# Kernel optimization log

Hardware: AMD Instinct MI355X
Metric: run time of the kernel (lower is better)

## Reference

```python
import jax, jax.numpy as jnp
import numpy as np

D_MODEL = 2048
N_HEADS = 16
D_KEY = D_MODEL // N_HEADS
ALIBI_SLOPE = 8.0
KEY_SCALE = D_KEY ** -0.5
B, S = 2, 2048


def setup_inputs() -> dict:
    key = jax.random.key(0)
    ks = jax.random.split(key, 12)
    sd = D_MODEL ** -0.5
    return {
        "states": jax.random.normal(ks[0], (B, S, D_MODEL), jnp.float32),
        "bias_mask": jax.random.normal(ks[1], (B, S, S), jnp.float32),
        # weights stored [in, out] (torch Linear applies x @ W.T + b)
        "wq": jax.random.normal(ks[2], (D_MODEL, D_MODEL), jnp.float32) * sd,
        "bq": jnp.zeros((D_MODEL,), jnp.float32),
        "wk": jax.random.normal(ks[3], (D_MODEL, D_MODEL), jnp.float32) * sd,
        "bk": jnp.zeros((D_MODEL,), jnp.float32),
        "wv": jax.random.normal(ks[4], (D_MODEL, D_MODEL), jnp.float32) * sd,
        "bv": jnp.zeros((D_MODEL,), jnp.float32),
        "wg": jax.random.normal(ks[5], (D_MODEL, N_HEADS), jnp.float32) * sd,
        "bg": jnp.zeros((N_HEADS,), jnp.float32),
        "wo": jax.random.normal(ks[6], (D_MODEL, D_MODEL), jnp.float32) * sd,
        "bo": jnp.zeros((D_MODEL,), jnp.float32),
    }


def reference(states, bias_mask, wq, bq, wk, bk, wv, bv, wg, bg, wo, bo):
    # head_scale = exp2(-(h+1)*alibi_slope/n_heads), non-trainable buffer
    head_scale = jnp.exp2(-(jnp.arange(N_HEADS, dtype=jnp.float32) + 1.0)
                          * ALIBI_SLOPE / N_HEADS)
    # [B, H, Q, K] bias with per-head ALiBi scaling
    bias = bias_mask[:, None, :, :] * head_scale[None, :, None, None]

    def heads(x, w, b):  # [B,S,D] -> [B,H,S,Dk]
        y = x @ w + b
        return y.reshape(x.shape[0], x.shape[1], N_HEADS, D_KEY).transpose(0, 2, 1, 3)

    q = heads(states, wq, bq)
    k = heads(states, wk, bk)
    v = heads(states, wv, bv)

    scores = jnp.einsum('bhqd,bhkd->bhqk', q, k) * KEY_SCALE + bias
    probs = jax.nn.softmax(scores, axis=-1)
    o = jnp.einsum('bhqk,bhkd->bqhd', probs, v)  # [B,S,H,Dk]

    g = jax.nn.sigmoid(states @ wg + bg)  # [B,S,H] head gate
    o = o * g[..., None]

    return o.reshape(o.shape[0], o.shape[1], D_MODEL) @ wo + bo
```

## Files before the change

### kernel.cpp

```cpp
#include <hip/hip_runtime.h>
#include <hip/hip_bf16.h>

#define SEQ 2048
#define DM 2048
#define NH 16
#define DK 128
#define LOG2E 1.4426950408889634f
#define QK_SCALE 0.08838834764831845f

typedef __attribute__((ext_vector_type(8))) short short8;
typedef __attribute__((ext_vector_type(4))) float f32x4;
typedef __attribute__((ext_vector_type(4))) unsigned short us4;

__device__ __forceinline__ unsigned short f2b(float f) {
  union { float f; unsigned u; } v; v.f = f;
  unsigned r = v.u + 0x7fffu + ((v.u >> 16) & 1u);
  return (unsigned short)(r >> 16);
}
__device__ __forceinline__ float b2f(unsigned short v) {
  union { unsigned u; float f; } x; x.u = ((unsigned)v) << 16; return x.f;
}

__device__ __forceinline__ void gl_lds16(const void* g, void* l) {
  __builtin_amdgcn_global_load_lds((const __attribute__((address_space(1))) void*)g,
                                   (__attribute__((address_space(3))) void*)l, 16, 0, 0);
}

#define SBAR()   __builtin_amdgcn_s_barrier()
#define SCHED0() __builtin_amdgcn_sched_barrier(0)
#define LGKM0()  asm volatile("s_waitcnt lgkmcnt(0)" ::: "memory")

__global__ __launch_bounds__(256) void cast2_bf16_kernel(const float* __restrict__ in0,
                                                         unsigned short* __restrict__ out0,
                                                         const float* __restrict__ in1,
                                                         unsigned short* __restrict__ out1) {
  int bid = blockIdx.x;
  const float* in = (bid < 4096) ? in0 : in1;
  unsigned short* out = (bid < 4096) ? out0 : out1;
  int i = ((bid < 4096) ? bid : bid - 4096) * 256 + threadIdx.x;
  const float4* p = (const float4*)in;
  float4 a = p[2*i], b = p[2*i+1];
  us4 r0, r1;
  r0[0]=f2b(a.x); r0[1]=f2b(a.y); r0[2]=f2b(a.z); r0[3]=f2b(a.w);
  r1[0]=f2b(b.x); r1[1]=f2b(b.y); r1[2]=f2b(b.z); r1[3]=f2b(b.w);
  us4* o = (us4*)out;
  o[2*i] = r0; o[2*i+1] = r1;
}

__global__ __launch_bounds__(256) void transpose_cast4_kernel(const float* __restrict__ w0,
                                                              const float* __restrict__ w1,
                                                              const float* __restrict__ w2,
                                                              const float* __restrict__ w3,
                                                              unsigned short* __restrict__ dst) {
  const float* w = (blockIdx.z == 0) ? w0 : (blockIdx.z == 1) ? w1 : (blockIdx.z == 2) ? w2 : w3;
  unsigned short* wt = dst + (size_t)blockIdx.z * DM * DM;
  __shared__ float t[64][65];
  int c0 = blockIdx.x * 64, r0 = blockIdx.y * 64;
  int tid = threadIdx.x;
  int rr = tid >> 4;
  int c4 = (tid & 15) * 4;
#pragma unroll
  for (int p = 0; p < 4; ++p) {
    int r = p*16 + rr;
    float4 v = *(const float4*)&w[(size_t)(r0 + r)*DM + c0 + c4];
    t[r][c4] = v.x; t[r][c4+1] = v.y; t[r][c4+2] = v.z; t[r][c4+3] = v.w;
  }
  __syncthreads();
#pragma unroll
  for (int p = 0; p < 4; ++p) {
    int c = p*16 + rr;
    us4 v;
    v[0] = f2b(t[c4+0][c]); v[1] = f2b(t[c4+1][c]);
    v[2] = f2b(t[c4+2][c]); v[3] = f2b(t[c4+3][c]);
    *(us4*)&wt[(size_t)(c0 + c)*DM + r0 + c4] = v;
  }
}

__global__ __launch_bounds__(256) void transpose_wg_kernel(const float* __restrict__ wg,
                                                           unsigned short* __restrict__ wgT) {
  int idx = blockIdx.x * 256 + threadIdx.x;
  int c = idx & 15;
  int r0 = (idx >> 4) * 4;
#pragma unroll
  for (int r = 0; r < 4; ++r)
    wgT[(size_t)c*DM + r0 + r] = f2b(wg[(size_t)(r0 + r)*NH + c]);
}

__device__ __forceinline__ void gemm128x128_core(const unsigned short* __restrict__ A,
                                                 const unsigned short* __restrict__ Bt,
                                                 int m0, int n0, f32x4 (&acc)[4][4]) {
  __shared__ __align__(16) unsigned short Ab[2][8192];
  __shared__ __align__(16) unsigned short Bb[2][8192];
  const int TK = DM / 64;

  int tid = threadIdx.x, wid = tid >> 6, lane = tid & 63;
  int lo = lane & 15, hi = lane >> 4;
  int wm = wid >> 1, wn = wid & 1;

  int srow8 = lane >> 3;
  int skb = (((lane & 7) ^ srow8) << 4);
  const char* Ag = (const char*)A;
  const char* Bg = (const char*)Bt;

#define STG_A(S,CUR) do {                                                          \
    const char* g = Ag + (size_t)(S)*128 + skb;                                    \
    char* l = (char*)&Ab[CUR][0] + wid*4096;                                       \
    _Pragma("unroll")                                                              \
    for (int c = 0; c < 4; ++c)                                                    \
      gl_lds16(g + (size_t)(m0 + wid*32 + c*8 + srow8)*4096, l + c*1024);          \
  } while(0)
#define STG_B(S,CUR) do {                                                          \
    const char* g = Bg + (size_t)(S)*128 + skb;                                    \
    char* l = (char*)&Bb[CUR][0] + wid*4096;                                       \
    _Pragma("unroll")                                                              \
    for (int c = 0; c < 4; ++c)                                                    \
      gl_lds16(g + (size_t)(n0 + wid*32 + c*8 + srow8)*4096, l + c*1024);          \
  } while(0)

#pragma unroll
  for (int i = 0; i < 4; ++i)
#pragma unroll
    for (int j = 0; j < 4; ++j) acc[i][j] = (f32x4){0.f,0.f,0.f,0.f};

  STG_B(0,0); STG_A(0,0); STG_B(1,1); STG_A(1,1);
  asm volatile("s_waitcnt vmcnt(8)" ::: "memory");
  SBAR();

  int msk = (lo & 7) << 4;
  int k0 = (hi*16) ^ msk;
  int k1 = (64 + hi*16) ^ msk;

  short8 a[4][2], bA[2][2], bB[2][2];

#define MF16(NHH,BF)                                                                \
  __builtin_amdgcn_s_setprio(1);                                                    \
  _Pragma("unroll") for (int mi = 0; mi < 4; ++mi)                                  \
  _Pragma("unroll") for (int nn = 0; nn < 2; ++nn) {                                \
    acc[mi][(NHH)*2+nn] = __builtin_amdgcn_mfma_f32_16x16x32_bf16(                  \
        a[mi][0], BF[nn][0], acc[mi][(NHH)*2+nn], 0, 0, 0);                         \
    acc[mi][(NHH)*2+nn] = __builtin_amdgcn_mfma_f32_16x16x32_bf16(                  \
        a[mi][1], BF[nn][1], acc[mi][(NHH)*2+nn], 0, 0, 0);                         \
  }                                                                                 \
  __builtin_amdgcn_s_setprio(0);

  for (int s = 0; s < TK; ++s) {
    int cur = s & 1;
    const char* Ac = (const char*)&Ab[cur][0];
    const char* Bc = (const char*)&Bb[cur][0];
    bool pre = (s + 2) < TK;

#pragma unroll
    for (int mm = 0; mm < 4; ++mm) {
      a[mm][0] = *(const short8*)(Ac + (wm*64 + mm*16 + lo)*128 + k0);
      a[mm][1] = *(const short8*)(Ac + (wm*64 + mm*16 + lo)*128 + k1);
    }
#pragma unroll
    for (int nn = 0; nn < 2; ++nn) {
      bA[nn][0] = *(const short8*)(Bc + (wn*64 + nn*16 + lo)*128 + k0);
      bA[nn][1] = *(const short8*)(Bc + (wn*64 + nn*16 + lo)*128 + k1);
      bB[nn][0] = *(const short8*)(Bc + (wn*64 + (2+nn)*16 + lo)*128 + k0);
      bB[nn][1] = *(const short8*)(Bc + (wn*64 + (2+nn)*16 + lo)*128 + k1);
    }
    SBAR(); LGKM0(); SCHED0();
    MF16(0, bA);
    SBAR();

    if (pre) {
      STG_B(s + 2, cur);
      STG_A(s + 2, cur);
      asm volatile("s_waitcnt vmcnt(8)" ::: "memory");
    } else if (s == TK - 2) {
      asm volatile("s_waitcnt vmcnt(0)" ::: "memory");
    }
    SBAR();
    MF16(1, bB);
    SBAR();
  }
#undef STG_A
#undef STG_B
#undef MF16
}

__global__ __launch_bounds__(256, 2) void gemm128_qkv_kernel(const unsigned short* __restrict__ A,
                                                             const unsigned short* __restrict__ Bt,
                                                             const float* __restrict__ bq,
                                                             const float* __restrict__ bk,
                                                             const float* __restrict__ bv,
                                                             unsigned short* __restrict__ QB,
                                                             unsigned short* __restrict__ KB,
                                                             unsigned short* __restrict__ VTB) {
  f32x4 acc[4][4];
  int n0 = blockIdx.x * 128, m0 = blockIdx.y * 128;
  gemm128x128_core(A, Bt, m0, n0, acc);

  int tid = threadIdx.x, wid = tid >> 6, lane = tid & 63;
  int lo = lane & 15, hi = lane >> 4;
  int wm = wid >> 1, wn = wid & 1;
  int m_base = m0 + wm*64;
  int n_base = n0 + wn*64;
  int sect = n0 >> 11;

  if (sect == 2) {
#pragma unroll
    for (int mi = 0; mi < 4; ++mi) {
      int m = m_base + mi*16 + 4*hi;
      int b = m >> 11, srow = m & 2047;
#pragma unroll
      for (int nf = 0; nf < 4; ++nf) {
        int n = n_base + nf*16 + lo;
        int nl = n & 2047, h = nl >> 7, d = nl & 127;
        float bvv = bv[nl];
        us4 pk;
#pragma unroll
        for (int r = 0; r < 4; ++r) pk[r] = f2b(acc[mi][nf][r] + bvv);
        *(us4*)&VTB[(((size_t)(b*NH + h))*DK + d)*SEQ + srow] = pk;
      }
    }
  } else {
    unsigned short* out = sect ? KB : QB;
    const float* bp = sect ? bk : bq;
    const float qs = sect ? 1.f : QK_SCALE * LOG2E;
#pragma unroll
    for (int mi = 0; mi < 4; ++mi) {
#pragma unroll
      for (int nf = 0; nf < 4; ++nf) {
        int n = n_base + nf*16 + lo;
        int nl = n & 2047, h = nl >> 7, d = nl & 127;
        float bvv = bp[nl];
#pragma unroll
        for (int r = 0; r < 4; ++r) {
          int m = m_base + mi*16 + 4*hi + r;
          int b = m >> 11, srow = m & 2047;
          out[(((size_t)(b*NH + h))*SEQ + srow)*DK + d] = f2b((acc[mi][nf][r] + bvv) * qs);
        }
      }
    }
  }
}

__global__ __launch_bounds__(256, 2) void gemm128_ao_kernel(const unsigned short* __restrict__ A,
                                                            const unsigned short* __restrict__ Bt,
                                                            const float* __restrict__ bias,
                                                            float* __restrict__ out) {
  f32x4 acc[4][4];
  int n0 = blockIdx.x * 128, m0 = blockIdx.y * 128;
  gemm128x128_core(A, Bt, m0, n0, acc);

  int tid = threadIdx.x, wid = tid >> 6, lane = tid & 63;
  int lo = lane & 15, hi = lane >> 4;
  int wm = wid >> 1, wn = wid & 1;
#pragma unroll
  for (int mi = 0; mi < 4; ++mi) {
#pragma unroll
    for (int nf = 0; nf < 4; ++nf) {
      int n = n0 + wn*64 + nf*16 + lo;
      float bvv = bias[n];
#pragma unroll
      for (int r = 0; r < 4; ++r) {
        int m = m0 + wm*64 + mi*16 + 4*hi + r;
        out[(size_t)m*DM + n] = acc[mi][nf][r] + bvv;
      }
    }
  }
}

__global__ __launch_bounds__(256) void gate_mfma_kernel(const unsigned short* __restrict__ XB,
                                                        const unsigned short* __restrict__ wgT,
                                                        const float* __restrict__ bg,
                                                        float* __restrict__ G) {
  int tid = threadIdx.x, wid = tid >> 6, lane = tid & 63;
  int lo = lane & 15, hi = lane >> 4;
  int m0 = blockIdx.x * 64 + wid * 16;

  f32x4 acc = {0.f, 0.f, 0.f, 0.f};
  const unsigned short* xrow = XB + (size_t)(m0 + lo) * DM + hi * 8;
  const unsigned short* grow = wgT + (size_t)lo * DM + hi * 8;
#pragma unroll 4
  for (int kt = 0; kt < DM; kt += 32) {
    short8 a = *(const short8*)(xrow + kt);
    short8 b = *(const short8*)(grow + kt);
    acc = __builtin_amdgcn_mfma_f32_16x16x32_bf16(a, b, acc, 0, 0, 0);
  }
  float bgv = bg[lo];
#pragma unroll
  for (int r = 0; r < 4; ++r) {
    float x = acc[r] + bgv;
    G[(size_t)(m0 + 4*hi + r) * NH + lo] = 1.f / (1.f + __builtin_amdgcn_exp2f(-x * LOG2E));
  }
}

__global__ __attribute__((amdgpu_flat_work_group_size(512,512)))
__attribute__((amdgpu_waves_per_eu(2,4)))
void attn_kernel(const unsigned short* __restrict__ Q,
                 const unsigned short* __restrict__ Kb,
                 const unsigned short* __restrict__ VT,
                 const unsigned short* __restrict__ biasb,
                 const float* __restrict__ G,
                 unsigned short* __restrict__ OG) {
  __shared__ __align__(16) unsigned short kbuf[2][64*128];
  __shared__ __align__(16) unsigned short vbuf[2][128*64];
  __shared__ __align__(16) unsigned short pbuf[8*16*64];

  int bid = blockIdx.x;
  int h  = bid & 15;
  int b  = (bid >> 4) & 1;
  int qt = bid >> 5;
  int bh = b*NH + h;

  int tid = threadIdx.x, wid = tid >> 6, lane = tid & 63;
  int lo = lane & 15, hi = lane >> 4;
  int qw0 = qt*256 + wid*32;

  float hs2 = __builtin_amdgcn_exp2f(-(float)(h+1) * 0.5f) * LOG2E;

  short8 qf[2][4];
#pragma unroll
  for (int f2 = 0; f2 < 2; ++f2)
#pragma unroll
    for (int ks = 0; ks < 4; ++ks)
      qf[f2][ks] = *(const short8*)&Q[((size_t)bh*SEQ + qw0 + f2*16 + lo)*DK + ks*32 + hi*8];

  f32x4 zero4 = {0.f,0.f,0.f,0.f};
  f32x4 acco[2][8];
#pragma unroll
  for (int f2 = 0; f2 < 2; ++f2)
#pragma unroll
    for (int f = 0; f < 8; ++f) acco[f2][f] = zero4;
  float lrun[2][4];
#pragma unroll
  for (int f2 = 0; f2 < 2; ++f2)
#pragma unroll
    for (int r = 0; r < 4; ++r) lrun[f2][r] = 0.f;

  const char* kbase = (const char*)Kb + ((size_t)bh*SEQ)*DK*2;
  const char* vbase = (const char*)VT + ((size_t)bh*DK)*SEQ*2;
  const unsigned short* bb = biasb + ((size_t)b*SEQ + qw0 + 4*hi)*SEQ + lo;
  char* pb = (char*)pbuf + wid*2048;

  int s16 = lane >> 4, srow8 = lane >> 3;
  int kof = (lane & 15) * 16, vof = (lane & 7) * 16;
  int w2 = wid * 2;

#define STAGE_KV(KT, BUF) do {                                                        \
    _Pragma("unroll")                                                                 \
    for (int c = 0; c < 2; ++c) {                                                     \
      int krc = (w2 + c)*4 + s16;                                                     \
      gl_lds16(kbase + (size_t)((KT) + krc)*256 + (kof ^ ((krc & 7) << 4)),           \
               (char*)kbuf[BUF] + (w2 + c)*1024);                                     \
      int vrc = (w2 + c)*8 + srow8;                                                   \
      gl_lds16(vbase + (size_t)vrc*4096 + (size_t)(KT)*2 + (vof ^ (srow8 << 4)),      \
               (char*)vbuf[BUF] + (w2 + c)*1024);                                     \
    }                                                                                 \
  } while(0)

  unsigned short br[2][4][4];
#pragma unroll
  for (int f2 = 0; f2 < 2; ++f2)
#pragma unroll
    for (int r = 0; r < 4; ++r)
#pragma unroll
      for (int nf = 0; nf < 4; ++nf)
        br[f2][r][nf] = bb[(size_t)(f2*16 + r)*SEQ + nf*16];
  STAGE_KV(0, 0);
  STAGE_KV(64, 1);
  asm volatile("s_waitcnt vmcnt(4)" ::: "memory");
  SBAR();

  const int NT = SEQ / 64;
  int cur = 0;
  for (int t = 0; t < NT; ++t) {
#pragma unroll
    for (int f2 = 0; f2 < 2; ++f2) {
      f32x4 sf[4];
      __builtin_amdgcn_s_setprio(1);
#pragma unroll
      for (int nf = 0; nf < 4; ++nf) {
        f32x4 a = zero4;
#pragma unroll
        for (int ks = 0; ks < 4; ++ks) {
          int krw = nf*16 + lo;
          int cb = (ks*32 + hi*8)*2;
          short8 kf = *(const short8*)((const char*)kbuf[cur] + krw*256 + (cb ^ ((krw & 7) << 4)));
          a = __builtin_amdgcn_mfma_f32_16x16x32_bf16(qf[f2][ks], kf, a, 0, 0, 0);
        }
        sf[nf] = a;
      }
      __builtin_amdgcn_s_setprio(0);

#pragma unroll
      for (int r = 0; r < 4; ++r) {
        int prow = 4*hi + r;
#pragma unroll
        for (int nf = 0; nf < 4; ++nf) {
          float s = fmaf(b2f(br[f2][r][nf]), hs2, sf[nf][r]);
          float p = __builtin_amdgcn_exp2f(s);
          lrun[f2][r] += p;
          *(unsigned short*)(pb + prow*128 + ((((nf*16 + lo)*2)) ^ ((prow & 7) << 4))) = f2b(p);
        }
      }

      short8 pf[2];
#pragma unroll
      for (int ks = 0; ks < 2; ++ks)
        pf[ks] = *(const short8*)(pb + lo*128 + ((ks*64 + hi*16) ^ ((lo & 7) << 4)));
      __builtin_amdgcn_s_setprio(1);
#pragma unroll
      for (int f = 0; f < 8; ++f) {
#pragma unroll
        for (int ks = 0; ks < 2; ++ks) {
          int vrw = f*16 + lo;
          int cb = (ks*32 + hi*8)*2;
          short8 vf = *(const short8*)((const char*)vbuf[cur] + vrw*128 + (cb ^ ((vrw & 7) << 4)));
          acco[f2][f] = __builtin_amdgcn_mfma_f32_16x16x32_bf16(pf[ks], vf, acco[f2][f], 0, 0, 0);
        }
      }
      __builtin_amdgcn_s_setprio(0);
    }

    LGKM0(); SBAR();

    bool more1 = (t + 1) < NT;
    bool more2 = (t + 2) < NT;
    if (more1) {
      int ktn = (t + 1) * 64;
#pragma unroll
      for (int f2 = 0; f2 < 2; ++f2)
#pragma unroll
        for (int r = 0; r < 4; ++r)
#pragma unroll
          for (int nf = 0; nf < 4; ++nf)
            br[f2][r][nf] = bb[(size_t)(f2*16 + r)*SEQ + ktn + nf*16];
    }
    if (more2) {
      STAGE_KV((t + 2) * 64, cur);
      asm volatile("s_waitcnt vmcnt(36)" ::: "memory");
    } else if (more1) {
      asm volatile("s_waitcnt vmcnt(32)" ::: "memory");
    }
    SBAR();
    cur ^= 1;
  }
#undef STAGE_KV

#pragma unroll
  for (int f2 = 0; f2 < 2; ++f2)
#pragma unroll
    for (int r = 0; r < 4; ++r) {
      float l = lrun[f2][r];
      l += __shfl_xor(l, 1); l += __shfl_xor(l, 2);
      l += __shfl_xor(l, 4); l += __shfl_xor(l, 8);
      lrun[f2][r] = l;
    }

#pragma unroll
  for (int f2 = 0; f2 < 2; ++f2)
#pragma unroll
    for (int r = 0; r < 4; ++r) {
      int qrow = qw0 + f2*16 + 4*hi + r;
      float inv = 1.f / lrun[f2][r];
      float g = G[((size_t)(b*SEQ + qrow))*NH + h];
      float sgl = inv * g;
#pragma unroll
      for (int f = 0; f < 8; ++f)
        OG[((size_t)(b*SEQ) + qrow)*DM + h*DK + f*16 + lo] = f2b(acco[f2][f][r] * sgl);
    }
}

extern "C" void kernel_launch(void* const* d_in, const int* in_sizes, int n_in,
                              void* d_out, int out_size, void* d_ws, size_t ws_size,
                              hipStream_t stream) {
  const float* states    = (const float*)d_in[0];
  const float* bias_mask = (const float*)d_in[1];
  const float* wq = (const float*)d_in[2];
  const float* bq = (const float*)d_in[3];
  const float* wk = (const float*)d_in[4];
  const float* bk = (const float*)d_in[5];
  const float* wv = (const float*)d_in[6];
  const float* bv = (const float*)d_in[7];
  const float* wg = (const float*)d_in[8];
  const float* bg = (const float*)d_in[9];
  const float* wo = (const float*)d_in[10];
  const float* bo = (const float*)d_in[11];

  char* ws = (char*)d_ws;
  unsigned short* XB   = (unsigned short*)(ws + 0);
  unsigned short* OGB  = XB;
  unsigned short* WQVT = (unsigned short*)(ws + 16777216UL);
  unsigned short* WOT  = (unsigned short*)(ws + 41943040UL);
  unsigned short* QB   = (unsigned short*)(ws + 50331648UL);
  unsigned short* KB   = (unsigned short*)(ws + 67108864UL);
  unsigned short* VTB  = (unsigned short*)(ws + 83886080UL);
  unsigned short* BIASB= (unsigned short*)(ws + 100663296UL);
  float*          GB   = (float*)         (ws + 117440512UL);
  unsigned short* WGT  = (unsigned short*)(ws + 117702656UL);

  cast2_bf16_kernel<<<8192, 256, 0, stream>>>(states, XB, bias_mask, BIASB);
  transpose_cast4_kernel<<<dim3(32, 32, 4), 256, 0, stream>>>(wq, wk, wv, wo, WQVT);
  transpose_wg_kernel<<<32, 256, 0, stream>>>(wg, WGT);

  gemm128_qkv_kernel<<<dim3(48, 32), 256, 0, stream>>>(XB, WQVT, bq, bk, bv, QB, KB, VTB);

  gate_mfma_kernel<<<64, 256, 0, stream>>>(XB, WGT, bg, GB);

  attn_kernel<<<256, 512, 0, stream>>>(QB, KB, VTB, BIASB, GB, OGB);

  gemm128_ao_kernel<<<dim3(16, 32), 256, 0, stream>>>(OGB, WOT, bo, (float*)d_out);
}
```

Baseline: 323.7 us.

## Halve attention query tile, single-buffer V, reuse K buffer for P

```diff
diff --git a/kernel.cpp b/kernel.cpp
--- a/kernel.cpp
+++ b/kernel.cpp
@@ -298,8 +298,7 @@
                  const float* __restrict__ G,
                  unsigned short* __restrict__ OG) {
   __shared__ __align__(16) unsigned short kbuf[2][64*128];
-  __shared__ __align__(16) unsigned short vbuf[2][128*64];
-  __shared__ __align__(16) unsigned short pbuf[8*16*64];
+  __shared__ __align__(16) unsigned short vbuf[128*64];
 
   int bid = blockIdx.x;
   int h  = bid & 15;
@@ -309,161 +308,156 @@
 
   int tid = threadIdx.x, wid = tid >> 6, lane = tid & 63;
   int lo = lane & 15, hi = lane >> 4;
-  int qw0 = qt*256 + wid*32;
+  int qw0 = qt*128 + wid*16;
 
   float hs2 = __builtin_amdgcn_exp2f(-(float)(h+1) * 0.5f) * LOG2E;
 
-  short8 qf[2][4];
-#pragma unroll
-  for (int f2 = 0; f2 < 2; ++f2)
-#pragma unroll
-    for (int ks = 0; ks < 4; ++ks)
-      qf[f2][ks] = *(const short8*)&Q[((size_t)bh*SEQ + qw0 + f2*16 + lo)*DK + ks*32 + hi*8];
+  short8 qf[4];
+#pragma unroll
+  for (int ks = 0; ks < 4; ++ks)
+    qf[ks] = *(const short8*)&Q[((size_t)bh*SEQ + qw0 + lo)*DK + ks*32 + hi*8];
 
   f32x4 zero4 = {0.f,0.f,0.f,0.f};
-  f32x4 acco[2][8];
-#pragma unroll
-  for (int f2 = 0; f2 < 2; ++f2)
-#pragma unroll
-    for (int f = 0; f < 8; ++f) acco[f2][f] = zero4;
-  float lrun[2][4];
-#pragma unroll
-  for (int f2 = 0; f2 < 2; ++f2)
-#pragma unroll
-    for (int r = 0; r < 4; ++r) lrun[f2][r] = 0.f;
+  f32x4 acco[8];
+#pragma unroll
+  for (int f = 0; f < 8; ++f) acco[f] = zero4;
+  float lrun[4];
+#pragma unroll
+  for (int r = 0; r < 4; ++r) lrun[r] = 0.f;
 
   const char* kbase = (const char*)Kb + ((size_t)bh*SEQ)*DK*2;
   const char* vbase = (const char*)VT + ((size_t)bh*DK)*SEQ*2;
   const unsigned short* bb = biasb + ((size_t)b*SEQ + qw0 + 4*hi)*SEQ + lo;
-  char* pb = (char*)pbuf + wid*2048;
 
   int s16 = lane >> 4, srow8 = lane >> 3;
   int kof = (lane & 15) * 16, vof = (lane & 7) * 16;
   int w2 = wid * 2;
 
-#define STAGE_KV(KT, BUF) do {                                                        \
+#define STAGE_K(KT, BUF) do {                                                         \
     _Pragma("unroll")                                                                 \
     for (int c = 0; c < 2; ++c) {                                                     \
       int krc = (w2 + c)*4 + s16;                                                     \
       gl_lds16(kbase + (size_t)((KT) + krc)*256 + (kof ^ ((krc & 7) << 4)),           \
                (char*)kbuf[BUF] + (w2 + c)*1024);                                     \
+    }                                                                                 \
+  } while(0)
+#define STAGE_V(KT) do {                                                              \
+    _Pragma("unroll")                                                                 \
+    for (int c = 0; c < 2; ++c) {                                                     \
       int vrc = (w2 + c)*8 + srow8;                                                   \
       gl_lds16(vbase + (size_t)vrc*4096 + (size_t)(KT)*2 + (vof ^ (srow8 << 4)),      \
-               (char*)vbuf[BUF] + (w2 + c)*1024);                                     \
+               (char*)vbuf + (w2 + c)*1024);                                          \
     }                                                                                 \
   } while(0)
 
-  unsigned short br[2][4][4];
-#pragma unroll
-  for (int f2 = 0; f2 < 2; ++f2)
-#pragma unroll
-    for (int r = 0; r < 4; ++r)
-#pragma unroll
-      for (int nf = 0; nf < 4; ++nf)
-        br[f2][r][nf] = bb[(size_t)(f2*16 + r)*SEQ + nf*16];
-  STAGE_KV(0, 0);
-  STAGE_KV(64, 1);
-  asm volatile("s_waitcnt vmcnt(4)" ::: "memory");
+  unsigned short br[4][4];
+  STAGE_V(0);
+#pragma unroll
+  for (int r = 0; r < 4; ++r)
+#pragma unroll
+    for (int nf = 0; nf < 4; ++nf)
+      br[r][nf] = bb[(size_t)r*SEQ + nf*16];
+  STAGE_K(0, 0);
+  STAGE_K(64, 1);
+  asm volatile("s_waitcnt vmcnt(2)" ::: "memory");
   SBAR();
 
   const int NT = SEQ / 64;
   int cur = 0;
   for (int t = 0; t < NT; ++t) {
-#pragma unroll
-    for (int f2 = 0; f2 < 2; ++f2) {
-      f32x4 sf[4];
-      __builtin_amdgcn_s_setprio(1);
+    f32x4 sf[4];
+    __builtin_amdgcn_s_setprio(1);
+#pragma unroll
+    for (int nf = 0; nf < 4; ++nf) {
+      f32x4 a = zero4;
+#pragma unroll
+      for (int ks = 0; ks < 4; ++ks) {
+        int krw = nf*16 + lo;
+        int cb = (ks*32 + hi*8)*2;
+        short8 kf = *(const short8*)((const char*)kbuf[cur] + krw*256 + (cb ^ ((krw & 7) << 4)));
+        a = __builtin_amdgcn_mfma_f32_16x16x32_bf16(qf[ks], kf, a, 0, 0, 0);
+      }
+      sf[nf] = a;
+    }
+    __builtin_amdgcn_s_setprio(0);
+
+    LGKM0();
+    asm volatile("s_waitcnt vmcnt(2)" ::: "memory");
+    SBAR();
+    char* pb = (char*)kbuf[cur] + wid*2048;
+
+#pragma unroll
+    for (int r = 0; r < 4; ++r) {
+      int prow = 4*hi + r;
 #pragma unroll
       for (int nf = 0; nf < 4; ++nf) {
-        f32x4 a = zero4;
-#pragma unroll
-        for (int ks = 0; ks < 4; ++ks) {
-          int krw = nf*16 + lo;
-          int cb = (ks*32 + hi*8)*2;
-          short8 kf = *(const short8*)((const char*)kbuf[cur] + krw*256 + (cb ^ ((krw & 7) << 4)));
-          a = __builtin_amdgcn_mfma_f32_16x16x32_bf16(qf[f2][ks], kf, a, 0, 0, 0);
-        }
-        sf[nf] = a;
+        float s = fmaf(b2f(br[r][nf]), hs2, sf[nf][r]);
+        float p = __builtin_amdgcn_exp2f(s);
+        lrun[r] += p;
+        *(unsigned short*)(pb + prow*128 + ((((nf*16 + lo)*2)) ^ ((prow & 7) << 4))) = f2b(p);
       }
-      __builtin_amdgcn_s_setprio(0);
-
-#pragma unroll
-      for (int r = 0; r < 4; ++r) {
-        int prow = 4*hi + r;
-#pragma unroll
-        for (int nf = 0; nf < 4; ++nf) {
-          float s = fmaf(b2f(br[f2][r][nf]), hs2, sf[nf][r]);
-          float p = __builtin_amdgcn_exp2f(s);
-          lrun[f2][r] += p;
-          *(unsigned short*)(pb + prow*128 + ((((nf*16 + lo)*2)) ^ ((prow & 7) << 4))) = f2b(p);
-        }
+    }
+
+    short8 pf[2];
+#pragma unroll
+    for (int ks = 0; ks < 2; ++ks)
+      pf[ks] = *(const short8*)(pb + lo*128 + ((ks*64 + hi*16) ^ ((lo & 7) << 4)));
+    __builtin_amdgcn_s_setprio(1);
+#pragma unroll
+    for (int f = 0; f < 8; ++f) {
+#pragma unroll
+      for (int ks = 0; ks < 2; ++ks) {
+        int vrw = f*16 + lo;
+        int cb = (ks*32 + hi*8)*2;
+        short8 vf = *(const short8*)((const char*)vbuf + vrw*128 + (cb ^ ((vrw & 7) << 4)));
+        acco[f] = __builtin_amdgcn_mfma_f32_16x16x32_bf16(pf[ks], vf, acco[f], 0, 0, 0);
       }
-
-      short8 pf[2];
-#pragma unroll
-      for (int ks = 0; ks < 2; ++ks)
-        pf[ks] = *(const short8*)(pb + lo*128 + ((ks*64 + hi*16) ^ ((lo & 7) << 4)));
-      __builtin_amdgcn_s_setprio(1);
-#pragma unroll
-      for (int f = 0; f < 8; ++f) {
-#pragma unroll
-        for (int ks = 0; ks < 2; ++ks) {
-          int vrw = f*16 + lo;
-          int cb = (ks*32 + hi*8)*2;
-          short8 vf = *(const short8*)((const char*)vbuf[cur] + vrw*128 + (cb ^ ((vrw & 7) << 4)));
-          acco[f2][f] = __builtin_amdgcn_mfma_f32_16x16x32_bf16(pf[ks], vf, acco[f2][f], 0, 0, 0);
-        }
-      }
-      __builtin_amdgcn_s_setprio(0);
-    }
+    }
+    __builtin_amdgcn_s_setprio(0);
 
     LGKM0(); SBAR();
 
     bool more1 = (t + 1) < NT;
     bool more2 = (t + 2) < NT;
     if (more1) {
+      STAGE_V((t + 1) * 64);
       int ktn = (t + 1) * 64;
 #pragma unroll
-      for (int f2 = 0; f2 < 2; ++f2)
-#pragma unroll
-        for (int r = 0; r < 4; ++r)
-#pragma unroll
-          for (int nf = 0; nf < 4; ++nf)
-            br[f2][r][nf] = bb[(size_t)(f2*16 + r)*SEQ + ktn + nf*16];
+      for (int r = 0; r < 4; ++r)
+#pragma unroll
+        for (int nf = 0; nf < 4; ++nf)
+          br[r][nf] = bb[(size_t)r*SEQ + ktn + nf*16];
     }
     if (more2) {
-      STAGE_KV((t + 2) * 64, cur);
-      asm volatile("s_waitcnt vmcnt(36)" ::: "memory");
+      STAGE_K((t + 2) * 64, cur);
+      asm volatile("s_waitcnt vmcnt(20)" ::: "memory");
     } else if (more1) {
-      asm volatile("s_waitcnt vmcnt(32)" ::: "memory");
+      asm volatile("s_waitcnt vmcnt(18)" ::: "memory");
     }
     SBAR();
     cur ^= 1;
   }
-#undef STAGE_KV
-
-#pragma unroll
-  for (int f2 = 0; f2 < 2; ++f2)
-#pragma unroll
-    for (int r = 0; r < 4; ++r) {
-      float l = lrun[f2][r];
-      l += __shfl_xor(l, 1); l += __shfl_xor(l, 2);
-      l += __shfl_xor(l, 4); l += __shfl_xor(l, 8);
-      lrun[f2][r] = l;
-    }
-
-#pragma unroll
-  for (int f2 = 0; f2 < 2; ++f2)
-#pragma unroll
-    for (int r = 0; r < 4; ++r) {
-      int qrow = qw0 + f2*16 + 4*hi + r;
-      float inv = 1.f / lrun[f2][r];
-      float g = G[((size_t)(b*SEQ + qrow))*NH + h];
-      float sgl = inv * g;
-#pragma unroll
-      for (int f = 0; f < 8; ++f)
-        OG[((size_t)(b*SEQ) + qrow)*DM + h*DK + f*16 + lo] = f2b(acco[f2][f][r] * sgl);
-    }
+#undef STAGE_K
+#undef STAGE_V
+
+#pragma unroll
+  for (int r = 0; r < 4; ++r) {
+    float l = lrun[r];
+    l += __shfl_xor(l, 1); l += __shfl_xor(l, 2);
+    l += __shfl_xor(l, 4); l += __shfl_xor(l, 8);
+    lrun[r] = l;
+  }
+
+#pragma unroll
+  for (int r = 0; r < 4; ++r) {
+    int qrow = qw0 + 4*hi + r;
+    float inv = 1.f / lrun[r];
+    float g = G[((size_t)(b*SEQ + qrow))*NH + h];
+    float sgl = inv * g;
+#pragma unroll
+    for (int f = 0; f < 8; ++f)
+      OG[((size_t)(b*SEQ) + qrow)*DM + h*DK + f*16 + lo] = f2b(acco[f][r] * sgl);
+  }
 }
 
 extern "C" void kernel_launch(void* const* d_in, const int* in_sizes, int n_in,
@@ -502,7 +496,7 @@
 
   gate_mfma_kernel<<<64, 256, 0, stream>>>(XB, WGT, bg, GB);
 
-  attn_kernel<<<256, 512, 0, stream>>>(QB, KB, VTB, BIASB, GB, OGB);
+  attn_kernel<<<512, 512, 0, stream>>>(QB, KB, VTB, BIASB, GB, OGB);
 
   gemm128_ao_kernel<<<dim3(16, 32), 256, 0, stream>>>(OGB, WOT, bo, (float*)d_out);
 }
```

New measurement: 351.3 us. 1.09x slower.
